# Performance work log

Measured on AMD Instinct MI355X. Metric: run time of the kernel, lower is better.

Reference implementation:

```python
import jax, jax.numpy as jnp
import numpy as np

EMBED = 1024
HEADS = 16
HEAD_DIM = EMBED // HEADS
MLP_DIM = 4096
EPS = 1e-5


def setup_inputs() -> dict:
    key = jax.random.key(0)
    ks = jax.random.split(key, 12)
    s = lambda d: 1.0 / np.sqrt(d)
    return {
        "x": jax.random.normal(ks[0], (8, 1024, EMBED), dtype=jnp.float32),
        "ln1_g": jnp.ones((EMBED,), jnp.float32),
        "ln1_b": jnp.zeros((EMBED,), jnp.float32),
        "w_qkv": jax.random.normal(ks[1], (EMBED, 3 * EMBED), jnp.float32) * s(EMBED),
        "b_qkv": jnp.zeros((3 * EMBED,), jnp.float32),
        "w_proj": jax.random.normal(ks[2], (EMBED, EMBED), jnp.float32) * s(EMBED),
        "b_proj": jnp.zeros((EMBED,), jnp.float32),
        "ln2_g": jnp.ones((EMBED,), jnp.float32),
        "ln2_b": jnp.zeros((EMBED,), jnp.float32),
        "w_fc1": jax.random.normal(ks[3], (EMBED, MLP_DIM), jnp.float32) * s(EMBED),
        "b_fc1": jnp.zeros((MLP_DIM,), jnp.float32),
        "w_fc2": jax.random.normal(ks[4], (MLP_DIM, EMBED), jnp.float32) * s(MLP_DIM),
        "b_fc2": jnp.zeros((EMBED,), jnp.float32),
    }


def _layernorm(x, g, b):
    mu = jnp.mean(x, axis=-1, keepdims=True)
    var = jnp.mean(jnp.square(x - mu), axis=-1, keepdims=True)
    return (x - mu) * jax.lax.rsqrt(var + EPS) * g + b


def reference(x, ln1_g, ln1_b, w_qkv, b_qkv, w_proj, b_proj,
              ln2_g, ln2_b, w_fc1, b_fc1, w_fc2, b_fc2):
    B, N, D = x.shape
    scale = HEAD_DIM ** -0.5

    # --- attention branch ---
    h = _layernorm(x, ln1_g, ln1_b)
    qkv = h @ w_qkv + b_qkv                       # [B,N,3D]
    qkv = qkv.reshape(B, N, 3, HEADS, HEAD_DIM)
    q, k, v = jnp.moveaxis(qkv, 2, 0)             # each [B,N,H,hd]
    attn = jnp.einsum('bqhd,bkhd->bhqk', q, k) * scale
    attn = jax.nn.softmax(attn, axis=-1)
    out = jnp.einsum('bhqk,bkhd->bqhd', attn, v).reshape(B, N, D)
    x = x + (out @ w_proj + b_proj)

    # --- MLP branch ---
    h = _layernorm(x, ln2_g, ln2_b)
    h = jax.nn.gelu(h @ w_fc1 + b_fc1, approximate=False)
    x = x + (h @ w_fc2 + b_fc2)
    return x
```

## Files before the change

### kernel.cpp

```cpp
#include <hip/hip_runtime.h>
#include <cstdint>


typedef unsigned short u16;
typedef short short8 __attribute__((ext_vector_type(8)));
typedef float floatx4 __attribute__((ext_vector_type(4)));

#define GLB(p) ((const __attribute__((address_space(1))) void*)(p))
#define LDSP(p) ((__attribute__((address_space(3))) void*)(p))

__device__ __forceinline__ u16 f2bf(float f) {
    uint32_t u = __float_as_uint(f);
    u += 0x7fffu + ((u >> 16) & 1u);
    return (u16)(u >> 16);
}

__global__ __launch_bounds__(256) void transpose_cast_kernel(
    const float* __restrict__ W, u16* __restrict__ Wt, int K, int N)
{
    __shared__ float tile[32][33];
    int n0 = blockIdx.x * 32, k0 = blockIdx.y * 32;
    int tx = threadIdx.x, ty = threadIdx.y;
    #pragma unroll
    for (int i = 0; i < 4; ++i)
        tile[ty + i * 8][tx] = W[(size_t)(k0 + ty + i * 8) * N + n0 + tx];
    __syncthreads();
    #pragma unroll
    for (int i = 0; i < 4; ++i)
        Wt[(size_t)(n0 + ty + i * 8) * K + k0 + tx] = f2bf(tile[tx][ty + i * 8]);
}

__global__ __launch_bounds__(256) void ln_kernel(
    const float* __restrict__ x, const float* __restrict__ gw,
    const float* __restrict__ bw, u16* __restrict__ out)
{
    const int row = blockIdx.x, tid = threadIdx.x;
    float4 v = ((const float4*)(x + (size_t)row * 1024))[tid];
    float s  = v.x + v.y + v.z + v.w;
    float ss = v.x * v.x + v.y * v.y + v.z * v.z + v.w * v.w;
    #pragma unroll
    for (int off = 32; off > 0; off >>= 1) {
        s  += __shfl_down(s, off);
        ss += __shfl_down(ss, off);
    }
    __shared__ float red[8];
    if ((tid & 63) == 0) { red[tid >> 6] = s; red[4 + (tid >> 6)] = ss; }
    __syncthreads();
    float S  = red[0] + red[1] + red[2] + red[3];
    float SS = red[4] + red[5] + red[6] + red[7];
    float mu  = S * (1.0f / 1024.0f);
    float var = SS * (1.0f / 1024.0f) - mu * mu;
    float rs  = rsqrtf(var + 1e-5f);
    float4 g4 = ((const float4*)gw)[tid];
    float4 b4 = ((const float4*)bw)[tid];
    u16* o = out + (size_t)row * 1024 + tid * 4;
    o[0] = f2bf((v.x - mu) * rs * g4.x + b4.x);
    o[1] = f2bf((v.y - mu) * rs * g4.y + b4.y);
    o[2] = f2bf((v.z - mu) * rs * g4.z + b4.z);
    o[3] = f2bf((v.w - mu) * rs * g4.w + b4.w);
}

#define MODE_BF16      0
#define MODE_BF16_GELU 1
#define MODE_F32_RES   2

template<int MODE>
__global__ __launch_bounds__(256) void gemm_bt_kernel(
    const u16* __restrict__ A, const u16* __restrict__ Bt,
    const float* __restrict__ bias, const float* __restrict__ res,
    void* __restrict__ outv, int M, int N, int K)
{
    __shared__ __attribute__((aligned(16))) u16 As[128 * 64];
    __shared__ __attribute__((aligned(16))) u16 Bs[128 * 64];
    const int tid = threadIdx.x;
    const int wave = tid >> 6, lane = tid & 63;
    const int lg = lane >> 4, lc = lane & 15;
    const int m0 = blockIdx.y * 128, n0 = blockIdx.x * 128;
    const int wr = wave >> 1, wc = wave & 1;

    floatx4 acc[4][4];
    #pragma unroll
    for (int i = 0; i < 4; ++i)
        #pragma unroll
        for (int j = 0; j < 4; ++j) acc[i][j] = floatx4{0.f, 0.f, 0.f, 0.f};

    const int srow = lane >> 3;
    const int schunk = (lane & 7) ^ srow;
    const u16* Ag = A  + (size_t)(m0 + wave * 32 + srow) * K + schunk * 8;
    const u16* Bg = Bt + (size_t)(n0 + wave * 32 + srow) * K + schunk * 8;
    u16* Asw = &As[wave * 4 * 512];
    u16* Bsw = &Bs[wave * 4 * 512];

    const int kiters = K >> 6;
    for (int kt = 0; kt < kiters; ++kt) {
        #pragma unroll
        for (int j = 0; j < 4; ++j) {
            __builtin_amdgcn_global_load_lds(GLB(Ag + (size_t)j * 8 * K), LDSP(Asw + j * 512), 16, 0, 0);
            __builtin_amdgcn_global_load_lds(GLB(Bg + (size_t)j * 8 * K), LDSP(Bsw + j * 512), 16, 0, 0);
        }
        Ag += 64; Bg += 64;
        __syncthreads();
        #pragma unroll
        for (int ks = 0; ks < 2; ++ks) {
            short8 fa[4], fb[4];
            #pragma unroll
            for (int mt = 0; mt < 4; ++mt)
                fa[mt] = *(const short8*)&As[(wr * 64 + mt * 16 + lc) * 64 +
                                             (((ks * 4 + lg) ^ (lc & 7)) * 8)];
            #pragma unroll
            for (int nt = 0; nt < 4; ++nt)
                fb[nt] = *(const short8*)&Bs[(wc * 64 + nt * 16 + lc) * 64 +
                                             (((ks * 4 + lg) ^ (lc & 7)) * 8)];
            #pragma unroll
            for (int mt = 0; mt < 4; ++mt)
                #pragma unroll
                for (int nt = 0; nt < 4; ++nt)
                    acc[mt][nt] = __builtin_amdgcn_mfma_f32_16x16x32_bf16(fa[mt], fb[nt], acc[mt][nt], 0, 0, 0);
        }
        __syncthreads();
    }

    #pragma unroll
    for (int mt = 0; mt < 4; ++mt) {
        #pragma unroll
        for (int nt = 0; nt < 4; ++nt) {
            const int col = n0 + wc * 64 + nt * 16 + lc;
            const float bv = bias[col];
            #pragma unroll
            for (int r = 0; r < 4; ++r) {
                const int row = m0 + wr * 64 + mt * 16 + lg * 4 + r;
                float v = acc[mt][nt][r] + bv;
                if (MODE == MODE_BF16) {
                    ((u16*)outv)[(size_t)row * N + col] = f2bf(v);
                } else if (MODE == MODE_BF16_GELU) {
                    float gl = 0.5f * v * (1.0f + erff(v * 0.70710678118f));
                    ((u16*)outv)[(size_t)row * N + col] = f2bf(gl);
                } else {
                    ((float*)outv)[(size_t)row * N + col] = v + res[(size_t)row * N + col];
                }
            }
        }
    }
}

__global__ __launch_bounds__(256) void attn_kernel(
    const u16* __restrict__ qkv, u16* __restrict__ out)
{
    const int blk = blockIdx.x;
    const int qt = blk & 15;
    const int h  = (blk >> 4) & 15;
    const int b  = blk >> 8;
    const int tid = threadIdx.x, wave = tid >> 6, lane = tid & 63;
    const int lg = lane >> 4, lc = lane & 15;

    __shared__ __attribute__((aligned(16))) u16 Qs[64 * 64];
    __shared__ __attribute__((aligned(16))) u16 Ks[64 * 64];
    __shared__ __attribute__((aligned(16))) u16 Vts[64 * 64];
    __shared__ __attribute__((aligned(16))) u16 Ps[64 * 64];

    const int q0 = qt * 64;
    const size_t hb = ((size_t)b * 1024) * 3072 + h * 64;
    const int srow = lane >> 3;
    const int schunk = (lane & 7) ^ srow;

    {
        const u16* Qg = qkv + hb + (size_t)(q0 + wave * 16 + srow) * 3072 + schunk * 8;
        u16* Qw = &Qs[wave * 2 * 512];
        __builtin_amdgcn_global_load_lds(GLB(Qg), LDSP(Qw), 16, 0, 0);
        __builtin_amdgcn_global_load_lds(GLB(Qg + (size_t)8 * 3072), LDSP(Qw + 512), 16, 0, 0);
    }
    __syncthreads();
    short8 aq[2];
    aq[0] = *(const short8*)&Qs[(wave * 16 + lc) * 64 + (((0 + lg) ^ (lc & 7)) * 8)];
    aq[1] = *(const short8*)&Qs[(wave * 16 + lc) * 64 + (((4 + lg) ^ (lc & 7)) * 8)];

    floatx4 o[4];
    #pragma unroll
    for (int dt = 0; dt < 4; ++dt) o[dt] = floatx4{0.f, 0.f, 0.f, 0.f};
    float mprev[4] = {-INFINITY, -INFINITY, -INFINITY, -INFINITY};
    float lsum[4]  = {0.f, 0.f, 0.f, 0.f};
    const float scale = 0.125f;

    for (int kt = 0; kt < 16; ++kt) {
        __syncthreads();
        {
            const u16* Kg = qkv + hb + 1024 +
                (size_t)(kt * 64 + wave * 16 + srow) * 3072 + schunk * 8;
            u16* Kw = &Ks[wave * 2 * 512];
            __builtin_amdgcn_global_load_lds(GLB(Kg), LDSP(Kw), 16, 0, 0);
            __builtin_amdgcn_global_load_lds(GLB(Kg + (size_t)8 * 3072), LDSP(Kw + 512), 16, 0, 0);
        }
        {
            const int key = tid >> 2, d0 = (tid & 3) * 16;
            const int kc = key >> 3, ke = key & 7;
            const uint4* vp = (const uint4*)(qkv + hb + 2048 + (size_t)(kt * 64 + key) * 3072 + d0);
            uint4 va = vp[0], vb = vp[1];
            u16 e[16];
            *(uint4*)(e) = va; *(uint4*)(e + 8) = vb;
            #pragma unroll
            for (int i = 0; i < 16; ++i) {
                const int d = d0 + i;
                Vts[d * 64 + ((kc ^ (d & 7)) * 8) + ke] = e[i];
            }
        }
        __syncthreads();

        floatx4 s[4];
        #pragma unroll
        for (int nt = 0; nt < 4; ++nt) s[nt] = floatx4{0.f, 0.f, 0.f, 0.f};
        #pragma unroll
        for (int ks = 0; ks < 2; ++ks)
            #pragma unroll
            for (int nt = 0; nt < 4; ++nt) {
                short8 fk = *(const short8*)&Ks[(nt * 16 + lc) * 64 +
                                                (((ks * 4 + lg) ^ (lc & 7)) * 8)];
                s[nt] = __builtin_amdgcn_mfma_f32_16x16x32_bf16(aq[ks], fk, s[nt], 0, 0, 0);
            }
        #pragma unroll
        for (int nt = 0; nt < 4; ++nt) s[nt] *= scale;

        float aexp[4];
        #pragma unroll
        for (int r = 0; r < 4; ++r) {
            float m = fmaxf(fmaxf(s[0][r], s[1][r]), fmaxf(s[2][r], s[3][r]));
            #pragma unroll
            for (int off = 8; off > 0; off >>= 1)
                m = fmaxf(m, __shfl_xor(m, off));
            float mn = fmaxf(mprev[r], m);
            aexp[r] = __expf(mprev[r] - mn);
            mprev[r] = mn;
        }
        float rs[4] = {0.f, 0.f, 0.f, 0.f};
        #pragma unroll
        for (int nt = 0; nt < 4; ++nt)
            #pragma unroll
            for (int r = 0; r < 4; ++r) {
                float p = __expf(s[nt][r] - mprev[r]);
                rs[r] += p;
                const int q = wave * 16 + lg * 4 + r;
                const int colc = nt * 2 + (lc >> 3);
                Ps[q * 64 + ((colc ^ (q & 7)) * 8) + (lc & 7)] = f2bf(p);
            }
        #pragma unroll
        for (int r = 0; r < 4; ++r) {
            #pragma unroll
            for (int off = 8; off > 0; off >>= 1)
                rs[r] += __shfl_xor(rs[r], off);
            lsum[r] = lsum[r] * aexp[r] + rs[r];
        }
        #pragma unroll
        for (int dt = 0; dt < 4; ++dt)
            #pragma unroll
            for (int r = 0; r < 4; ++r)
                o[dt][r] *= aexp[r];
        __syncthreads();

        #pragma unroll
        for (int ks = 0; ks < 2; ++ks) {
            short8 ap = *(const short8*)&Ps[(wave * 16 + lc) * 64 +
                                            (((ks * 4 + lg) ^ (lc & 7)) * 8)];
            #pragma unroll
            for (int dt = 0; dt < 4; ++dt) {
                short8 fv = *(const short8*)&Vts[(dt * 16 + lc) * 64 +
                                                 (((ks * 4 + lg) ^ (lc & 7)) * 8)];
                o[dt] = __builtin_amdgcn_mfma_f32_16x16x32_bf16(ap, fv, o[dt], 0, 0, 0);
            }
        }
    }

    #pragma unroll
    for (int dt = 0; dt < 4; ++dt)
        #pragma unroll
        for (int r = 0; r < 4; ++r) {
            const int q = q0 + wave * 16 + lg * 4 + r;
            float val = o[dt][r] / lsum[r];
            out[((size_t)b * 1024 + q) * 1024 + h * 64 + dt * 16 + lc] = f2bf(val);
        }
}

extern "C" void kernel_launch(void* const* d_in, const int* in_sizes, int n_in,
                              void* d_out, int out_size, void* d_ws, size_t ws_size,
                              hipStream_t stream)
{
    const float* x      = (const float*)d_in[0];
    const float* ln1_g  = (const float*)d_in[1];
    const float* ln1_b  = (const float*)d_in[2];
    const float* w_qkv  = (const float*)d_in[3];
    const float* b_qkv  = (const float*)d_in[4];
    const float* w_proj = (const float*)d_in[5];
    const float* b_proj = (const float*)d_in[6];
    const float* ln2_g  = (const float*)d_in[7];
    const float* ln2_b  = (const float*)d_in[8];
    const float* w_fc1  = (const float*)d_in[9];
    const float* b_fc1  = (const float*)d_in[10];
    const float* w_fc2  = (const float*)d_in[11];
    const float* b_fc2  = (const float*)d_in[12];
    float* outp = (float*)d_out;

    char* ws = (char*)d_ws;
    size_t off = 0;
    auto alloc = [&](size_t bytes) { void* p = ws + off; off += (bytes + 255) & ~(size_t)255; return p; };
    u16*  wqkvT  = (u16*)alloc((size_t)3072 * 1024 * 2);
    u16*  wprojT = (u16*)alloc((size_t)1024 * 1024 * 2);
    u16*  wfc1T  = (u16*)alloc((size_t)4096 * 1024 * 2);
    u16*  wfc2T  = (u16*)alloc((size_t)1024 * 4096 * 2);
    u16*  hbuf   = (u16*)alloc((size_t)8192 * 1024 * 2);
    u16*  big    = (u16*)alloc((size_t)8192 * 4096 * 2);
    u16*  attno  = (u16*)alloc((size_t)8192 * 1024 * 2);
    float* x2    = (float*)alloc((size_t)8192 * 1024 * 4);

    dim3 tb(32, 8);
    transpose_cast_kernel<<<dim3(3072 / 32, 1024 / 32), tb, 0, stream>>>(w_qkv,  wqkvT,  1024, 3072);
    transpose_cast_kernel<<<dim3(1024 / 32, 1024 / 32), tb, 0, stream>>>(w_proj, wprojT, 1024, 1024);
    transpose_cast_kernel<<<dim3(4096 / 32, 1024 / 32), tb, 0, stream>>>(w_fc1,  wfc1T,  1024, 4096);
    transpose_cast_kernel<<<dim3(1024 / 32, 4096 / 32), tb, 0, stream>>>(w_fc2,  wfc2T,  4096, 1024);

    ln_kernel<<<8192, 256, 0, stream>>>(x, ln1_g, ln1_b, hbuf);
    gemm_bt_kernel<MODE_BF16><<<dim3(3072 / 128, 8192 / 128), 256, 0, stream>>>(
        hbuf, wqkvT, b_qkv, nullptr, big, 8192, 3072, 1024);
    attn_kernel<<<2048, 256, 0, stream>>>(big, attno);
    gemm_bt_kernel<MODE_F32_RES><<<dim3(1024 / 128, 8192 / 128), 256, 0, stream>>>(
        attno, wprojT, b_proj, x, x2, 8192, 1024, 1024);
    ln_kernel<<<8192, 256, 0, stream>>>(x2, ln2_g, ln2_b, hbuf);
    gemm_bt_kernel<MODE_BF16_GELU><<<dim3(4096 / 128, 8192 / 128), 256, 0, stream>>>(
        hbuf, wfc1T, b_fc1, nullptr, big, 8192, 4096, 1024);
    gemm_bt_kernel<MODE_F32_RES><<<dim3(1024 / 128, 8192 / 128), 256, 0, stream>>>(
        big, wfc2T, b_fc2, x2, outp, 8192, 1024, 4096);
}
```

Before: 572.9 us.

## Write transposed V from QKV GEMM epilogue and restructure attention with transposed scores

The QKV GEMM epilogue now writes V directly in a per-batch transposed [d, token] layout, so the attention kernel can load V tiles with async global-to-LDS copies instead of an element-by-element scalar transpose each iteration. Attention computes S^T (K as the A operand), so each lane owns one query row. That cuts the softmax reductions to two cross-lane shuffles, lets P and the output be written as packed bf16 pairs, and removes the barrier before the PV MMA. Block indexing is also remapped so that neighbouring blocks group batch-head pairs, which may improve K/V cache reuse. The cost is an extra 16 MB V buffer and a wasted write of V into the qkv buffer is skipped, which introduces cross-kernel layout coupling.

Result: faster. 518.4 us (-9.5%).

```diff
diff --git a/kernel.cpp b/kernel.cpp
--- a/kernel.cpp
+++ b/kernel.cpp
@@ -13,6 +13,9 @@
     uint32_t u = __float_as_uint(f);
     u += 0x7fffu + ((u >> 16) & 1u);
     return (u16)(u >> 16);
+}
+__device__ __forceinline__ uint32_t pack2(float a, float b) {
+    return (uint32_t)f2bf(a) | ((uint32_t)f2bf(b) << 16);
 }
 
 __global__ __launch_bounds__(256) void transpose_cast_kernel(
@@ -63,12 +66,13 @@
 #define MODE_BF16      0
 #define MODE_BF16_GELU 1
 #define MODE_F32_RES   2
+#define MODE_QKV       3
 
 template<int MODE>
 __global__ __launch_bounds__(256) void gemm_bt_kernel(
     const u16* __restrict__ A, const u16* __restrict__ Bt,
     const float* __restrict__ bias, const float* __restrict__ res,
-    void* __restrict__ outv, int M, int N, int K)
+    void* __restrict__ outv, u16* __restrict__ vt, int M, int N, int K)
 {
     __shared__ __attribute__((aligned(16))) u16 As[128 * 64];
     __shared__ __attribute__((aligned(16))) u16 Bs[128 * 64];
@@ -120,6 +124,24 @@
         __syncthreads();
     }
 
+    if (MODE == MODE_QKV && n0 >= 2048) {
+        #pragma unroll
+        for (int mt = 0; mt < 4; ++mt) {
+            #pragma unroll
+            for (int nt = 0; nt < 4; ++nt) {
+                const int col = n0 + wc * 64 + nt * 16 + lc;
+                const float bv = bias[col];
+                const int hd = col - 2048;
+                const int rowbase = m0 + wr * 64 + mt * 16 + lg * 4;
+                const int b = rowbase >> 10, token = rowbase & 1023;
+                float v0 = acc[mt][nt][0] + bv, v1 = acc[mt][nt][1] + bv;
+                float v2 = acc[mt][nt][2] + bv, v3 = acc[mt][nt][3] + bv;
+                uint2 pk = {pack2(v0, v1), pack2(v2, v3)};
+                *(uint2*)&vt[((size_t)b * 1024 + hd) * 1024 + token] = pk;
+            }
+        }
+        return;
+    }
     #pragma unroll
     for (int mt = 0; mt < 4; ++mt) {
         #pragma unroll
@@ -130,7 +152,7 @@
             for (int r = 0; r < 4; ++r) {
                 const int row = m0 + wr * 64 + mt * 16 + lg * 4 + r;
                 float v = acc[mt][nt][r] + bv;
-                if (MODE == MODE_BF16) {
+                if (MODE == MODE_BF16 || MODE == MODE_QKV) {
                     ((u16*)outv)[(size_t)row * N + col] = f2bf(v);
                 } else if (MODE == MODE_BF16_GELU) {
                     float gl = 0.5f * v * (1.0f + erff(v * 0.70710678118f));
@@ -144,12 +166,12 @@
 }
 
 __global__ __launch_bounds__(256) void attn_kernel(
-    const u16* __restrict__ qkv, u16* __restrict__ out)
-{
-    const int blk = blockIdx.x;
-    const int qt = blk & 15;
-    const int h  = (blk >> 4) & 15;
-    const int b  = blk >> 8;
+    const u16* __restrict__ qkv, const u16* __restrict__ vtg, u16* __restrict__ out)
+{
+    const int bid = blockIdx.x;
+    const int g = ((bid >> 7) << 3) | (bid & 7);
+    const int qt = (bid >> 3) & 15;
+    const int h = g & 15, b = g >> 4;
     const int tid = threadIdx.x, wave = tid >> 6, lane = tid & 63;
     const int lg = lane >> 4, lc = lane & 15;
 
@@ -160,12 +182,13 @@
 
     const int q0 = qt * 64;
     const size_t hb = ((size_t)b * 1024) * 3072 + h * 64;
+    const u16* vhead = vtg + ((size_t)b * 1024 + h * 64) * 1024;
     const int srow = lane >> 3;
     const int schunk = (lane & 7) ^ srow;
 
     {
         const u16* Qg = qkv + hb + (size_t)(q0 + wave * 16 + srow) * 3072 + schunk * 8;
-        u16* Qw = &Qs[wave * 2 * 512];
+        u16* Qw = &Qs[wave * 1024];
         __builtin_amdgcn_global_load_lds(GLB(Qg), LDSP(Qw), 16, 0, 0);
         __builtin_amdgcn_global_load_lds(GLB(Qg + (size_t)8 * 3072), LDSP(Qw + 512), 16, 0, 0);
     }
@@ -177,105 +200,90 @@
     floatx4 o[4];
     #pragma unroll
     for (int dt = 0; dt < 4; ++dt) o[dt] = floatx4{0.f, 0.f, 0.f, 0.f};
-    float mprev[4] = {-INFINITY, -INFINITY, -INFINITY, -INFINITY};
-    float lsum[4]  = {0.f, 0.f, 0.f, 0.f};
-    const float scale = 0.125f;
+    float mprev = -INFINITY, lsum = 0.f;
+    const float sc = 0.125f;
 
     for (int kt = 0; kt < 16; ++kt) {
         __syncthreads();
         {
             const u16* Kg = qkv + hb + 1024 +
                 (size_t)(kt * 64 + wave * 16 + srow) * 3072 + schunk * 8;
-            u16* Kw = &Ks[wave * 2 * 512];
+            u16* Kw = &Ks[wave * 1024];
             __builtin_amdgcn_global_load_lds(GLB(Kg), LDSP(Kw), 16, 0, 0);
             __builtin_amdgcn_global_load_lds(GLB(Kg + (size_t)8 * 3072), LDSP(Kw + 512), 16, 0, 0);
         }
         {
-            const int key = tid >> 2, d0 = (tid & 3) * 16;
-            const int kc = key >> 3, ke = key & 7;
-            const uint4* vp = (const uint4*)(qkv + hb + 2048 + (size_t)(kt * 64 + key) * 3072 + d0);
-            uint4 va = vp[0], vb = vp[1];
-            u16 e[16];
-            *(uint4*)(e) = va; *(uint4*)(e + 8) = vb;
-            #pragma unroll
-            for (int i = 0; i < 16; ++i) {
-                const int d = d0 + i;
-                Vts[d * 64 + ((kc ^ (d & 7)) * 8) + ke] = e[i];
-            }
+            const u16* Vg = vhead + (size_t)(wave * 16 + srow) * 1024 + kt * 64 + schunk * 8;
+            u16* Vw = &Vts[wave * 1024];
+            __builtin_amdgcn_global_load_lds(GLB(Vg), LDSP(Vw), 16, 0, 0);
+            __builtin_amdgcn_global_load_lds(GLB(Vg + (size_t)8 * 1024), LDSP(Vw + 512), 16, 0, 0);
         }
         __syncthreads();
 
-        floatx4 s[4];
-        #pragma unroll
-        for (int nt = 0; nt < 4; ++nt) s[nt] = floatx4{0.f, 0.f, 0.f, 0.f};
+        floatx4 st[4];
+        #pragma unroll
+        for (int nt = 0; nt < 4; ++nt) st[nt] = floatx4{0.f, 0.f, 0.f, 0.f};
         #pragma unroll
         for (int ks = 0; ks < 2; ++ks)
             #pragma unroll
             for (int nt = 0; nt < 4; ++nt) {
                 short8 fk = *(const short8*)&Ks[(nt * 16 + lc) * 64 +
                                                 (((ks * 4 + lg) ^ (lc & 7)) * 8)];
-                s[nt] = __builtin_amdgcn_mfma_f32_16x16x32_bf16(aq[ks], fk, s[nt], 0, 0, 0);
+                st[nt] = __builtin_amdgcn_mfma_f32_16x16x32_bf16(fk, aq[ks], st[nt], 0, 0, 0);
             }
-        #pragma unroll
-        for (int nt = 0; nt < 4; ++nt) s[nt] *= scale;
-
-        float aexp[4];
-        #pragma unroll
-        for (int r = 0; r < 4; ++r) {
-            float m = fmaxf(fmaxf(s[0][r], s[1][r]), fmaxf(s[2][r], s[3][r]));
-            #pragma unroll
-            for (int off = 8; off > 0; off >>= 1)
-                m = fmaxf(m, __shfl_xor(m, off));
-            float mn = fmaxf(mprev[r], m);
-            aexp[r] = __expf(mprev[r] - mn);
-            mprev[r] = mn;
-        }
-        float rs[4] = {0.f, 0.f, 0.f, 0.f};
+
+        float m = st[0][0];
         #pragma unroll
         for (int nt = 0; nt < 4; ++nt)
             #pragma unroll
-            for (int r = 0; r < 4; ++r) {
-                float p = __expf(s[nt][r] - mprev[r]);
-                rs[r] += p;
-                const int q = wave * 16 + lg * 4 + r;
-                const int colc = nt * 2 + (lc >> 3);
-                Ps[q * 64 + ((colc ^ (q & 7)) * 8) + (lc & 7)] = f2bf(p);
-            }
-        #pragma unroll
-        for (int r = 0; r < 4; ++r) {
-            #pragma unroll
-            for (int off = 8; off > 0; off >>= 1)
-                rs[r] += __shfl_xor(rs[r], off);
-            lsum[r] = lsum[r] * aexp[r] + rs[r];
-        }
+            for (int r = 0; r < 4; ++r) m = fmaxf(m, st[nt][r]);
+        m = fmaxf(m, __shfl_xor(m, 16));
+        m = fmaxf(m, __shfl_xor(m, 32));
+        float mn = fmaxf(mprev, m * sc);
+        float aexp = __expf(mprev - mn);
+        mprev = mn;
+
+        const int q = wave * 16 + lc;
+        float rs = 0.f;
+        #pragma unroll
+        for (int nt = 0; nt < 4; ++nt) {
+            float p0 = __expf(st[nt][0] * sc - mn);
+            float p1 = __expf(st[nt][1] * sc - mn);
+            float p2 = __expf(st[nt][2] * sc - mn);
+            float p3 = __expf(st[nt][3] * sc - mn);
+            rs += (p0 + p1) + (p2 + p3);
+            const int c16 = nt * 2 + (lg >> 1);
+            uint2 pk = {pack2(p0, p1), pack2(p2, p3)};
+            *(uint2*)&Ps[q * 64 + ((c16 ^ (lc & 7)) * 8) + (lg & 1) * 4] = pk;
+        }
+        rs += __shfl_xor(rs, 16);
+        rs += __shfl_xor(rs, 32);
+        lsum = lsum * aexp + rs;
         #pragma unroll
         for (int dt = 0; dt < 4; ++dt)
             #pragma unroll
-            for (int r = 0; r < 4; ++r)
-                o[dt][r] *= aexp[r];
-        __syncthreads();
+            for (int r = 0; r < 4; ++r) o[dt][r] *= aexp;
 
         #pragma unroll
         for (int ks = 0; ks < 2; ++ks) {
-            short8 ap = *(const short8*)&Ps[(wave * 16 + lc) * 64 +
-                                            (((ks * 4 + lg) ^ (lc & 7)) * 8)];
+            short8 fp = *(const short8*)&Ps[q * 64 + (((ks * 4 + lg) ^ (lc & 7)) * 8)];
             #pragma unroll
             for (int dt = 0; dt < 4; ++dt) {
                 short8 fv = *(const short8*)&Vts[(dt * 16 + lc) * 64 +
                                                  (((ks * 4 + lg) ^ (lc & 7)) * 8)];
-                o[dt] = __builtin_amdgcn_mfma_f32_16x16x32_bf16(ap, fv, o[dt], 0, 0, 0);
+                o[dt] = __builtin_amdgcn_mfma_f32_16x16x32_bf16(fv, fp, o[dt], 0, 0, 0);
             }
         }
     }
 
-    #pragma unroll
-    for (int dt = 0; dt < 4; ++dt)
-        #pragma unroll
-        for (int r = 0; r < 4; ++r) {
-            const int q = q0 + wave * 16 + lg * 4 + r;
-            float val = o[dt][r] / lsum[r];
-            out[((size_t)b * 1024 + q) * 1024 + h * 64 + dt * 16 + lc] = f2bf(val);
-        }
+    const float rl = 1.0f / lsum;
+    const int q = q0 + wave * 16 + lc;
+    #pragma unroll
+    for (int dt = 0; dt < 4; ++dt) {
+        uint2 pk = {pack2(o[dt][0] * rl, o[dt][1] * rl),
+                    pack2(o[dt][2] * rl, o[dt][3] * rl)};
+        *(uint2*)&out[((size_t)b * 1024 + q) * 1024 + h * 64 + dt * 16 + lg * 4] = pk;
+    }
 }
 
 extern "C" void kernel_launch(void* const* d_in, const int* in_sizes, int n_in,
@@ -306,6 +314,7 @@
     u16*  wfc2T  = (u16*)alloc((size_t)1024 * 4096 * 2);
     u16*  hbuf   = (u16*)alloc((size_t)8192 * 1024 * 2);
     u16*  big    = (u16*)alloc((size_t)8192 * 4096 * 2);
+    u16*  vtbuf  = (u16*)alloc((size_t)8 * 1024 * 1024 * 2);
     u16*  attno  = (u16*)alloc((size_t)8192 * 1024 * 2);
     float* x2    = (float*)alloc((size_t)8192 * 1024 * 4);
 
@@ -316,14 +325,14 @@
     transpose_cast_kernel<<<dim3(1024 / 32, 4096 / 32), tb, 0, stream>>>(w_fc2,  wfc2T,  4096, 1024);
 
     ln_kernel<<<8192, 256, 0, stream>>>(x, ln1_g, ln1_b, hbuf);
-    gemm_bt_kernel<MODE_BF16><<<dim3(3072 / 128, 8192 / 128), 256, 0, stream>>>(
-        hbuf, wqkvT, b_qkv, nullptr, big, 8192, 3072, 1024);
-    attn_kernel<<<2048, 256, 0, stream>>>(big, attno);
+    gemm_bt_kernel<MODE_QKV><<<dim3(3072 / 128, 8192 / 128), 256, 0, stream>>>(
+        hbuf, wqkvT, b_qkv, nullptr, big, vtbuf, 8192, 3072, 1024);
+    attn_kernel<<<2048, 256, 0, stream>>>(big, vtbuf, attno);
     gemm_bt_kernel<MODE_F32_RES><<<dim3(1024 / 128, 8192 / 128), 256, 0, stream>>>(
-        attno, wprojT, b_proj, x, x2, 8192, 1024, 1024);
+        attno, wprojT, b_proj, x, x2, nullptr, 8192, 1024, 1024);
     ln_kernel<<<8192, 256, 0, stream>>>(x2, ln2_g, ln2_b, hbuf);
     gemm_bt_kernel<MODE_BF16_GELU><<<dim3(4096 / 128, 8192 / 128), 256, 0, stream>>>(
-        hbuf, wfc1T, b_fc1, nullptr, big, 8192, 4096, 1024);
+        hbuf, wfc1T, b_fc1, nullptr, big, nullptr, 8192, 4096, 1024);
     gemm_bt_kernel<MODE_F32_RES><<<dim3(1024 / 128, 8192 / 128), 256, 0, stream>>>(
-        big, wfc2T, b_fc2, x2, outp, 8192, 1024, 4096);
-}
+        big, wfc2T, b_fc2, x2, outp, nullptr, 8192, 1024, 4096);
+}
```
